# Performance work log

Hardware: AMD Instinct MI355X
Metric: run time of the kernel (lower is better)

The kernel has to match this reference:

```python
import jax, jax.numpy as jnp
import numpy as np

N_NODES = 100_000
N_EDGES = 1_000_000
H = 128
NUM_STATES = 4
UPPER_T, LOWER_T, NUM_ITERS, TEMP_EVAL = 1.0, 0.1, 10000, 0.1


def temp_by_step(step, upper, lower, num_iters, temp_eval):
    # Python-level schedule: eval temp at step == -1, else linear anneal.
    if step == -1:
        return temp_eval
    frac = min(step / num_iters, 1.0)
    return upper + (lower - upper) * frac


def from_binary_states(states):
    # [*, k] bits -> integer id in [0, 2**k)
    weights = 2 ** jnp.arange(states.shape[-1])
    return (states * weights).sum(-1)


def setup_inputs() -> dict:
    key = jax.random.key(0)
    ks = jax.random.split(key, 20)
    N, E, h = N_NODES, N_EDGES, H
    node_states = jax.random.randint(ks[0], (N, NUM_STATES), 0, 2)
    edge_states = jax.random.randint(ks[1], (E, NUM_STATES), 0, 2)
    scalars = jax.random.normal(ks[2], (E, 1), jnp.float32)
    # first N edges are self-loops ordered by node id (required by the module's
    # node_scalars = scalars[src == dst] indexing convention)
    loops = jnp.arange(N)
    src = jax.random.randint(ks[3], (E - N,), 0, N)
    dst = jax.random.randint(ks[4], (E - N,), 0, N)
    dst = jnp.where(dst == src, (dst + 1) % N, dst)  # no accidental self-loops
    edge_index = jnp.stack([jnp.concatenate([loops, src]),
                            jnp.concatenate([loops, dst])])
    batched_reverse_idx = jax.random.randint(ks[5], (E,), 0, E)
    batch_scalars = jax.random.normal(ks[6], (E, 1, 1), jnp.float32)
    s = 0.02
    params = dict(
        node_emb=s * jax.random.normal(ks[7], (2 ** NUM_STATES, h), jnp.float32),
        edge_emb=s * jax.random.normal(ks[8], (2 ** NUM_STATES, h), jnp.float32),
        combine_W=s * jax.random.normal(ks[9], (2 * h, h), jnp.float32),
        combine_b=jnp.zeros((h,), jnp.float32),
        keep_W=s * jax.random.normal(ks[10], (h, 2), jnp.float32),
        keep_b=jnp.zeros((2,), jnp.float32),
        push_W=s * jax.random.normal(ks[11], (h, 2), jnp.float32),
        push_b=jnp.zeros((2,), jnp.float32),
        push_node_W=s * jax.random.normal(ks[12], (h, 2), jnp.float32),
        push_node_b=jnp.zeros((2,), jnp.float32),
        increment_W=s * jax.random.normal(ks[13], (h, 2), jnp.float32),
        increment_b=jnp.zeros((2,), jnp.float32),
    )
    return dict(node_states=node_states, edge_states=edge_states, scalars=scalars,
                edge_index=edge_index, batched_reverse_idx=batched_reverse_idx,
                batch_scalars=batch_scalars, processor_step=0, training_step=0,
                **params)


def reference(node_states, edge_states, scalars, edge_index, batched_reverse_idx,
              batch_scalars, processor_step, training_step,
              node_emb, edge_emb, combine_W, combine_b, keep_W, keep_b,
              push_W, push_b, push_node_W, push_node_b,
              increment_W, increment_b):
    N = node_states.shape[0]
    tau = temp_by_step(int(training_step), UPPER_T, LOWER_T, NUM_ITERS, TEMP_EVAL)
    # use_noise = config.use_noise (False) and training_step != -1 -> False

    node_fts = node_emb[from_binary_states(node_states)]   # [N, h]
    edge_fts = edge_emb[from_binary_states(edge_states)]   # [E, h]
    src, dst = edge_index[0], edge_index[1]
    fts = jnp.concatenate([edge_fts[batched_reverse_idx], node_fts[src]], axis=1)
    fts = fts @ combine_W + combine_b                       # [E, h]

    s = scalars.reshape(-1)                                 # [E]

    def pair_gumbel_first(W, b):
        # grouped (per-edge pair) softmax; take first component (== [::2])
        logits = (fts @ W + b) / tau                        # [E, 2]
        return jax.nn.softmax(logits, axis=-1)[:, 0]

    increment = 1.0 * pair_gumbel_first(increment_W, increment_b)
    keep = s * pair_gumbel_first(keep_W, keep_b)

    # push: first N edges are self-loops, self-loop of node i is edge i
    push_wo = pair_gumbel_first(push_W, push_b)
    push_w = pair_gumbel_first(push_node_W, push_node_b)
    node_scalars = s[:N]                                    # scalars at self-loops
    s_wo = s - node_scalars[dst]
    s_w = s_wo + node_scalars[src]
    acc = (jax.ops.segment_sum(push_wo * s_wo, dst, num_segments=N)
           + jax.ops.segment_sum(push_w * s_w, dst, num_segments=N))  # [N]
    edge_push = jnp.zeros_like(s).at[:N].set(acc)           # nonzero only on self-loops

    new_scalars = (increment + keep + edge_push)[:, None]   # [E, 1]
    target = batch_scalars[:, processor_step]               # [E, 1]
    loss = jnp.mean((target - new_scalars) ** 2)
    return new_scalars, loss
```

## Files before the change

kernel.cpp:

```cpp
#include <hip/hip_runtime.h>
#include <math.h>
#include <stdint.h>

#define N_NODES 100000
#define N_EDGES 1000000
#define N_NONLOOP (N_EDGES - N_NODES)
#define NXCD 8

#define ACC_SCALE   1048576.0f
#define ACC_INV     (1.0f / 1048576.0f)

typedef float  vfloat4 __attribute__((ext_vector_type(4)));
typedef int    vint4   __attribute__((ext_vector_type(4)));

#define XCC_ID_HWREG (20 | ((4 - 1) << 11))

__device__ __forceinline__ int get_xcc() {
    return __builtin_amdgcn_s_getreg(XCC_ID_HWREG) & (NXCD - 1);
}

__device__ __forceinline__ void l2_atomic_add_u32(uint32_t* p, uint32_t v) {
    asm volatile("global_atomic_add %0, %1, off" :: "v"(p), "v"(v) : "memory");
}
__device__ __forceinline__ void l2_atomic_add_f32(float* p, float v) {
    asm volatile("global_atomic_add_f32 %0, %1, off" :: "v"(p), "v"(v) : "memory");
}

__device__ __forceinline__ float get_invtau(const int* __restrict__ training_step) {
    int step = training_step[0];
    float tau;
    if (step == -1) {
        tau = 0.1f;
    } else {
        float frac = fminf((float)step / 10000.0f, 1.0f);
        tau = 1.0f + (0.1f - 1.0f) * frac;
    }
    return 1.0f / tau;
}

__device__ __forceinline__ float wave_reduce(float v) {
    #pragma unroll
    for (int off = 32; off > 0; off >>= 1) v += __shfl_down(v, off, 64);
    return v;
}

#define TAB_BLOCKS  132
#define NODE_BLOCKS 391
#define EI_BLOCKS   977

__global__ __launch_bounds__(256) void fused_pre(
    const int* __restrict__ node_states,
    const int* __restrict__ edge_states,
    const float* __restrict__ node_emb,
    const float* __restrict__ edge_emb,
    const float* __restrict__ cW, const float* __restrict__ cb,
    const float* __restrict__ kW, const float* __restrict__ kb,
    const float* __restrict__ pW, const float* __restrict__ pb,
    const float* __restrict__ pnW, const float* __restrict__ pnb,
    const float* __restrict__ iW, const float* __restrict__ ib,
    const int* __restrict__ tstep,
    uint32_t* __restrict__ acc,
    uint8_t* __restrict__ ei,
    uint8_t* __restrict__ nib,
    float* __restrict__ tabs,
    float* __restrict__ lossp,
    float* __restrict__ loss_out,
    int ncopies)
{
    const int b = blockIdx.x;

    if (b < TAB_BLOCKS) {
        const int w    = b;
        const int lane = threadIdx.x & 63;
        const int wv   = threadIdx.x >> 6;
        const float invtau = get_invtau(tstep);
        __shared__ float part[4];

        float p = 0.f;
        if (w < 128) {
            const int isB = w >> 6, h = (w >> 4) & 3, i = w & 15;
            const float* emb = isB ? node_emb : edge_emb;
            const float* cWh = cW + isB * 128 * 128;
            float t0 = 0.f, t1 = 0.f;
            const int l0 = wv * 32;
            #pragma unroll 8
            for (int l = l0; l < l0 + 32; ++l) {
                const float el = emb[i * 128 + l];
                t0 += el * cWh[l * 128 + lane];
                t1 += el * cWh[l * 128 + 64 + lane];
            }
            const float* W = (h == 0) ? kW : (h == 1) ? pW : (h == 2) ? pnW : iW;
            const float wd0 = W[2 * lane] - W[2 * lane + 1];
            const float wd1 = W[2 * (lane + 64)] - W[2 * (lane + 64) + 1];
            p = t0 * wd0 + t1 * wd1;
        } else if (wv == 0) {
            const int h = w & 3;
            const float* W = (h == 0) ? kW : (h == 1) ? pW : (h == 2) ? pnW : iW;
            const float wd0 = W[2 * lane] - W[2 * lane + 1];
            const float wd1 = W[2 * (lane + 64)] - W[2 * (lane + 64) + 1];
            p = cb[lane] * wd0 + cb[64 + lane] * wd1;
        }
        p = wave_reduce(p);
        if (lane == 0) part[wv] = p;
        __syncthreads();
        if (threadIdx.x == 0) {
            const float tot = part[0] + part[1] + part[2] + part[3];
            if (w < 128) {
                const int isB = w >> 6, h = (w >> 4) & 3, i = w & 15;
                tabs[isB * 64 + i * 4 + h] = tot * invtau;
            } else {
                const int h = w & 3;
                const float* bb = (h == 0) ? kb : (h == 1) ? pb : (h == 2) ? pnb : ib;
                tabs[128 + h] = (tot + bb[0] - bb[1]) * invtau;
            }
        }
        return;
    }

    if (b < TAB_BLOCKS + NODE_BLOCKS) {
        const int n = (b - TAB_BLOCKS) * 256 + threadIdx.x;
        if (n < 256) lossp[n] = 0.f;
        if (n == 0) *loss_out = 0.f;
        if (n < N_NODES) {
            vint4 st = __builtin_nontemporal_load(&((const vint4*)node_states)[n]);
            nib[n] = (uint8_t)(st.x + 2 * st.y + 4 * st.z + 8 * st.w);
            for (int k = 0; k < ncopies; ++k) acc[(size_t)k * N_NODES + n] = 0u;
        }
        return;
    }

    const int t = (b - TAB_BLOCKS - NODE_BLOCKS) * 256 + threadIdx.x;
    if (t < N_EDGES / 4) {
        const vint4* esp = (const vint4*)edge_states + 4 * t;
        vint4 e0 = __builtin_nontemporal_load(esp + 0);
        vint4 e1 = __builtin_nontemporal_load(esp + 1);
        vint4 e2 = __builtin_nontemporal_load(esp + 2);
        vint4 e3 = __builtin_nontemporal_load(esp + 3);
        const uint32_t i0 = e0.x + 2 * e0.y + 4 * e0.z + 8 * e0.w;
        const uint32_t i1 = e1.x + 2 * e1.y + 4 * e1.z + 8 * e1.w;
        const uint32_t i2 = e2.x + 2 * e2.y + 4 * e2.z + 8 * e2.w;
        const uint32_t i3 = e3.x + 2 * e3.y + 4 * e3.z + 8 * e3.w;
        ((uint32_t*)ei)[t] = i0 | (i1 << 8) | (i2 << 16) | (i3 << 24);
    }
}

template<int MODE>
__global__ __launch_bounds__(256) void edge_kernel(
    const float* __restrict__ s,
    const int* __restrict__ src,
    const int* __restrict__ dst,
    const int* __restrict__ brev,
    const uint8_t* __restrict__ ei,
    const uint8_t* __restrict__ nib,
    const float* __restrict__ tabs,
    const float* __restrict__ target,
    uint32_t* __restrict__ acc,
    float* __restrict__ lossp,
    float* __restrict__ out,
    float* __restrict__ loss_out)
{
    __shared__ float4 sf[MODE ? 160 : 33];
    if (threadIdx.x < 33) sf[threadIdx.x] = ((const float4*)tabs)[threadIdx.x];
    __syncthreads();

    int xcc = 0;
    uint32_t* accx = acc;
    if (MODE == 1) {
        xcc  = get_xcc();
        accx = acc + (size_t)xcc * N_NODES;
    }

    const int t = blockIdx.x * blockDim.x + threadIdx.x;
    const bool active = (t < N_NONLOOP / 4);
    float lsum = 0.f;
    float ov[4];
    int   iv[4];
    int   dsv[4];
    int   g = 0;

    if (active) {
        g = (N_NODES / 4) + t;
        const vint4   rv = __builtin_nontemporal_load(&((const vint4*)brev)[g]);
        const vint4   sr = __builtin_nontemporal_load(&((const vint4*)src)[g]);
        const vint4   ds = __builtin_nontemporal_load(&((const vint4*)dst)[g]);
        const vfloat4 sv = __builtin_nontemporal_load(&((const vfloat4*)s)[g]);
        const vfloat4 tg = __builtin_nontemporal_load(&((const vfloat4*)target)[g]);

        const int rvv[4] = {rv.x, rv.y, rv.z, rv.w};
        const int srv[4] = {sr.x, sr.y, sr.z, sr.w};
        dsv[0] = ds.x; dsv[1] = ds.y; dsv[2] = ds.z; dsv[3] = ds.w;
        const float svv[4] = {sv.x, sv.y, sv.z, sv.w};
        const float tgv[4] = {tg.x, tg.y, tg.z, tg.w};

        int   eidx[4], ni[4];
        float ss[4], sd[4];
        #pragma unroll
        for (int j = 0; j < 4; ++j) {
            eidx[j] = ei[rvv[j]];
            ni[j]   = nib[srv[j]];
            ss[j]   = s[srv[j]];
            sd[j]   = s[dsv[j]];
        }

        const float4 c4 = sf[32];
        #pragma unroll
        for (int j = 0; j < 4; ++j) {
            const float4 a = sf[eidx[j]];
            const float4 b = sf[16 + ni[j]];
            const float lk  = a.x + b.x + c4.x;
            const float lp  = a.y + b.y + c4.y;
            const float lpn = a.z + b.z + c4.z;
            const float li  = a.w + b.w + c4.w;
            const float pk  = 1.f / (1.f + __expf(-lk));
            const float pp  = 1.f / (1.f + __expf(-lp));
            const float ppn = 1.f / (1.f + __expf(-lpn));
            const float pi  = 1.f / (1.f + __expf(-li));

            const float s_wo = svv[j] - sd[j];
            const float s_w  = s_wo + ss[j];
            iv[j] = __float2int_rn((pp * s_wo + ppn * s_w) * ACC_SCALE);

            ov[j] = pi + svv[j] * pk;
            const float d = tgv[j] - ov[j];
            lsum += d * d;
        }
    }

    lsum = wave_reduce(lsum);
    __shared__ float wsum[4];
    const int lane = threadIdx.x & 63, wid = threadIdx.x >> 6;
    if (lane == 0) wsum[wid] = lsum;
    __syncthreads();
    if (threadIdx.x == 0) {
        const float tot = (wsum[0] + wsum[1] + wsum[2] + wsum[3]) * (1.0f / (float)N_EDGES);
        if (MODE == 1) l2_atomic_add_f32(&lossp[xcc * 32], tot);
        else           atomicAdd(loss_out, tot);
    }

    if (active) {
        #pragma unroll
        for (int j = 0; j < 4; ++j) {
            if (MODE == 1) l2_atomic_add_u32(&accx[dsv[j]], (uint32_t)iv[j]);
            else           atomicAdd((unsigned int*)&acc[dsv[j]], (unsigned int)iv[j]);
        }
        vfloat4 o4 = {ov[0], ov[1], ov[2], ov[3]};
        __builtin_nontemporal_store(o4, &((vfloat4*)out)[g]);
    }
}

template<int NC>
__global__ __launch_bounds__(256) void finalize_nodes(
    const float* __restrict__ s,
    const int* __restrict__ brev,
    const uint8_t* __restrict__ ei,
    const uint8_t* __restrict__ nib,
    const float* __restrict__ tabs,
    const float* __restrict__ target,
    const uint32_t* __restrict__ acc,
    const float* __restrict__ lossp,
    float* __restrict__ out,
    float* __restrict__ loss_out)
{
    __shared__ float4 sf[33];
    if (threadIdx.x < 33) sf[threadIdx.x] = ((const float4*)tabs)[threadIdx.x];
    __syncthreads();

    const int n = blockIdx.x * blockDim.x + threadIdx.x;
    const bool active = (n < N_NODES);
    float sq = 0.f, v = 0.f;
    if (active) {
        const int  eidx = ei[brev[n]];
        const int  ni   = nib[n];
        const float sv  = s[n];

        uint32_t asum = 0u;
        #pragma unroll
        for (int k = 0; k < NC; ++k) asum += acc[(size_t)k * N_NODES + n];
        const float a8 = (float)(int)asum * ACC_INV;

        const float4 a  = sf[eidx];
        const float4 b  = sf[16 + ni];
        const float4 c4 = sf[32];
        const float lk  = a.x + b.x + c4.x;
        const float lpn = a.z + b.z + c4.z;
        const float li  = a.w + b.w + c4.w;
        const float pk  = 1.f / (1.f + __expf(-lk));
        const float ppn = 1.f / (1.f + __expf(-lpn));
        const float pi  = 1.f / (1.f + __expf(-li));

        v = pi + sv * (pk + ppn) + a8;
        const float d = target[n] - v;
        sq = d * d;
    }
    sq = wave_reduce(sq);
    __shared__ float wsum[4];
    const int lane = threadIdx.x & 63, wid = threadIdx.x >> 6;
    if (lane == 0) wsum[wid] = sq;
    __syncthreads();
    if (threadIdx.x == 0) {
        float tot = (wsum[0] + wsum[1] + wsum[2] + wsum[3]) * (1.0f / (float)N_EDGES);
        if (blockIdx.x == 0) {
            #pragma unroll
            for (int k = 0; k < NXCD; ++k) tot += lossp[k * 32];
        }
        atomicAdd(loss_out, tot);
    }
    if (active) out[n] = v;
}

extern "C" void kernel_launch(void* const* d_in, const int* in_sizes, int n_in,
                              void* d_out, int out_size, void* d_ws, size_t ws_size,
                              hipStream_t stream) {
    const int*   node_states   = (const int*)d_in[0];
    const int*   edge_states   = (const int*)d_in[1];
    const float* scalars       = (const float*)d_in[2];
    const int*   edge_index    = (const int*)d_in[3];
    const int*   brev          = (const int*)d_in[4];
    const float* batch_scalars = (const float*)d_in[5];
    const int*   training_step = (const int*)d_in[7];
    const float* node_emb  = (const float*)d_in[8];
    const float* edge_emb  = (const float*)d_in[9];
    const float* combine_W = (const float*)d_in[10];
    const float* combine_b = (const float*)d_in[11];
    const float* keep_W  = (const float*)d_in[12];
    const float* keep_b  = (const float*)d_in[13];
    const float* push_W  = (const float*)d_in[14];
    const float* push_b  = (const float*)d_in[15];
    const float* pushn_W = (const float*)d_in[16];
    const float* pushn_b = (const float*)d_in[17];
    const float* inc_W   = (const float*)d_in[18];
    const float* inc_b   = (const float*)d_in[19];

    float* out = (float*)d_out;

    const size_t need_scoped = 2048 + (size_t)NXCD * N_NODES * 4 + N_EDGES + N_NODES;
    const bool scoped = (ws_size >= need_scoped);
    const int nc = scoped ? NXCD : 1;

    char* ws = (char*)d_ws;
    float*    tabs  = (float*)ws;
    float*    lossp = (float*)(ws + 1024);
    uint32_t* acc   = (uint32_t*)(ws + 2048);
    uint8_t*  ei    = (uint8_t*)(ws + 2048 + (size_t)nc * N_NODES * 4);
    uint8_t*  nib   = ei + N_EDGES;

    const int* srcp = edge_index;
    const int* dstp = edge_index + N_EDGES;

    fused_pre<<<TAB_BLOCKS + NODE_BLOCKS + EI_BLOCKS, 256, 0, stream>>>(
        node_states, edge_states, node_emb, edge_emb,
        combine_W, combine_b, keep_W, keep_b, push_W, push_b,
        pushn_W, pushn_b, inc_W, inc_b, training_step,
        acc, ei, nib, tabs, lossp, out + N_EDGES, nc);

    const int ethreads = N_NONLOOP / 4;
    const int eblocks  = (ethreads + 255) / 256;
    if (scoped) {
        edge_kernel<1><<<eblocks, 256, 0, stream>>>(
            scalars, srcp, dstp, brev, ei, nib, tabs, batch_scalars,
            acc, lossp, out, out + N_EDGES);
        finalize_nodes<NXCD><<<(N_NODES + 255) / 256, 256, 0, stream>>>(
            scalars, brev, ei, nib, tabs, batch_scalars, acc, lossp, out, out + N_EDGES);
    } else {
        edge_kernel<0><<<eblocks, 256, 0, stream>>>(
            scalars, srcp, dstp, brev, ei, nib, tabs, batch_scalars,
            acc, lossp, out, out + N_EDGES);
        finalize_nodes<1><<<(N_NODES + 255) / 256, 256, 0, stream>>>(
            scalars, brev, ei, nib, tabs, batch_scalars, acc, lossp, out, out + N_EDGES);
    }
}
```

Baseline: 174.6 us.

## Replace global scatter atomics with partitioned binning and LDS accumulation

Instead of fixed-point global atomics into per-XCD accumulator copies, the edge kernel groups each edge's push contribution by destination partition (8 ranges of 12500 nodes). It appends (local index, value) pairs to per-partition buffers using block-level histogram offsets. A new bin_accum kernel accumulates each partition chunk with LDS float atomics into per-block partial rows, and the finalize kernel sums 8 partials per node. This aims to remove contended L2 atomics, at the cost of extra writes and reads of the pair buffer and partials, one more launch, a hard per-partition capacity that silently drops overflow, and a new large workspace requirement; the path only runs if the workspace is big enough.

```diff
diff --git a/kernel.cpp b/kernel.cpp
--- a/kernel.cpp
+++ b/kernel.cpp
@@ -7,18 +7,23 @@
 #define N_NONLOOP (N_EDGES - N_NODES)
 #define NXCD 8
 
+#define NP    8
+#define PSZ   12500
+#define PCAP  120000
+#define GOWN  8
+#define PROW  12544
+
 #define ACC_SCALE   1048576.0f
 #define ACC_INV     (1.0f / 1048576.0f)
 
 typedef float  vfloat4 __attribute__((ext_vector_type(4)));
 typedef int    vint4   __attribute__((ext_vector_type(4)));
+typedef unsigned long long u64;
 
 #define XCC_ID_HWREG (20 | ((4 - 1) << 11))
-
 __device__ __forceinline__ int get_xcc() {
     return __builtin_amdgcn_s_getreg(XCC_ID_HWREG) & (NXCD - 1);
 }
-
 __device__ __forceinline__ void l2_atomic_add_u32(uint32_t* p, uint32_t v) {
     asm volatile("global_atomic_add %0, %1, off" :: "v"(p), "v"(v) : "memory");
 }
@@ -60,6 +65,7 @@
     const float* __restrict__ iW, const float* __restrict__ ib,
     const int* __restrict__ tstep,
     uint32_t* __restrict__ acc,
+    uint32_t* __restrict__ cnt,
     uint8_t* __restrict__ ei,
     uint8_t* __restrict__ nib,
     float* __restrict__ tabs,
@@ -121,6 +127,9 @@
         const int n = (b - TAB_BLOCKS) * 256 + threadIdx.x;
         if (n < 256) lossp[n] = 0.f;
         if (n == 0) *loss_out = 0.f;
+        if (ncopies == 0) {
+            if (n < NP) cnt[n] = 0u;
+        }
         if (n < N_NODES) {
             vint4 st = __builtin_nontemporal_load(&((const vint4*)node_states)[n]);
             nib[n] = (uint8_t)(st.x + 2 * st.y + 4 * st.z + 8 * st.w);
@@ -142,6 +151,201 @@
         const uint32_t i3 = e3.x + 2 * e3.y + 4 * e3.z + 8 * e3.w;
         ((uint32_t*)ei)[t] = i0 | (i1 << 8) | (i2 << 16) | (i3 << 24);
     }
+}
+
+__global__ __launch_bounds__(256) void edge_compact(
+    const float* __restrict__ s,
+    const int* __restrict__ src,
+    const int* __restrict__ dst,
+    const int* __restrict__ brev,
+    const uint8_t* __restrict__ ei,
+    const uint8_t* __restrict__ nib,
+    const float* __restrict__ tabs,
+    const float* __restrict__ target,
+    uint32_t* __restrict__ cnt,
+    u64* __restrict__ pairs,
+    float* __restrict__ lossp,
+    float* __restrict__ out)
+{
+    __shared__ float4 sf[33];
+    __shared__ uint32_t hist[NP], lbase[NP], loff[NP];
+    const int tid = threadIdx.x;
+    if (tid < 33) sf[tid] = ((const float4*)tabs)[tid];
+    if (tid < NP) { hist[tid] = 0u; loff[tid] = 0u; }
+    __syncthreads();
+
+    const int t = blockIdx.x * 256 + tid;
+    const bool active = (t < N_NONLOOP / 4);
+    float lsum = 0.f;
+    float ov[4], av[4];
+    int   pj[4], dloc[4];
+    int   g = 0;
+
+    if (active) {
+        g = (N_NODES / 4) + t;
+        const vint4   rv = __builtin_nontemporal_load(&((const vint4*)brev)[g]);
+        const vint4   sr = __builtin_nontemporal_load(&((const vint4*)src)[g]);
+        const vint4   ds = __builtin_nontemporal_load(&((const vint4*)dst)[g]);
+        const vfloat4 sv = __builtin_nontemporal_load(&((const vfloat4*)s)[g]);
+        const vfloat4 tg = __builtin_nontemporal_load(&((const vfloat4*)target)[g]);
+
+        const int rvv[4] = {rv.x, rv.y, rv.z, rv.w};
+        const int srv[4] = {sr.x, sr.y, sr.z, sr.w};
+        const int dsv[4] = {ds.x, ds.y, ds.z, ds.w};
+        const float svv[4] = {sv.x, sv.y, sv.z, sv.w};
+        const float tgv[4] = {tg.x, tg.y, tg.z, tg.w};
+
+        int   eidx[4], ni[4];
+        float ss[4], sd[4];
+        #pragma unroll
+        for (int j = 0; j < 4; ++j) {
+            eidx[j] = ei[rvv[j]];
+            ni[j]   = nib[srv[j]];
+            ss[j]   = s[srv[j]];
+            sd[j]   = s[dsv[j]];
+        }
+
+        const float4 c4 = sf[32];
+        #pragma unroll
+        for (int j = 0; j < 4; ++j) {
+            const float4 a = sf[eidx[j]];
+            const float4 b = sf[16 + ni[j]];
+            const float lk  = a.x + b.x + c4.x;
+            const float lp  = a.y + b.y + c4.y;
+            const float lpn = a.z + b.z + c4.z;
+            const float li  = a.w + b.w + c4.w;
+            const float pk  = 1.f / (1.f + __expf(-lk));
+            const float pp  = 1.f / (1.f + __expf(-lp));
+            const float ppn = 1.f / (1.f + __expf(-lpn));
+            const float pi  = 1.f / (1.f + __expf(-li));
+
+            const float s_wo = svv[j] - sd[j];
+            const float s_w  = s_wo + ss[j];
+            av[j] = pp * s_wo + ppn * s_w;
+
+            const uint32_t p = (uint32_t)dsv[j] / 12500u;
+            pj[j]   = (int)p;
+            dloc[j] = dsv[j] - (int)p * 12500;
+
+            ov[j] = pi + svv[j] * pk;
+            const float d = tgv[j] - ov[j];
+            lsum += d * d;
+        }
+        #pragma unroll
+        for (int j = 0; j < 4; ++j) atomicAdd(&hist[pj[j]], 1u);
+    }
+
+    __syncthreads();
+    if (tid < NP) lbase[tid] = atomicAdd(&cnt[tid], hist[tid]);
+    __syncthreads();
+
+    if (active) {
+        #pragma unroll
+        for (int j = 0; j < 4; ++j) {
+            const uint32_t k    = atomicAdd(&loff[pj[j]], 1u);
+            const uint32_t slot = lbase[pj[j]] + k;
+            if (slot < PCAP)
+                pairs[(size_t)pj[j] * PCAP + slot] =
+                    ((u64)(uint32_t)dloc[j] << 32) | (uint32_t)__float_as_int(av[j]);
+        }
+        vfloat4 o4 = {ov[0], ov[1], ov[2], ov[3]};
+        __builtin_nontemporal_store(o4, &((vfloat4*)out)[g]);
+    }
+
+    lsum = wave_reduce(lsum);
+    if ((tid & 63) == 0)
+        atomicAdd(&lossp[(blockIdx.x & 15) * 16], lsum);
+}
+
+__global__ __launch_bounds__(256) void bin_accum(
+    const u64* __restrict__ pairs,
+    const uint32_t* __restrict__ cnt,
+    float* __restrict__ partials)
+{
+    __shared__ float part[PSZ];
+    const int tid = threadIdx.x;
+    const int p = blockIdx.x >> 3, r = blockIdx.x & 7;
+
+    for (int k = tid; k < PSZ; k += 256) part[k] = 0.f;
+    __syncthreads();
+
+    uint32_t c = cnt[p];
+    if (c > PCAP) c = PCAP;
+    const uint32_t chunk = (c + GOWN - 1) / GOWN;
+    const uint32_t lo = r * chunk;
+    uint32_t hi = lo + chunk;
+    if (hi > c) hi = c;
+
+    const u64* pp = pairs + (size_t)p * PCAP;
+    for (uint32_t i = lo + tid; i < hi; i += 256) {
+        const u64 v = pp[i];
+        atomicAdd(&part[(uint32_t)(v >> 32)], __int_as_float((int)(uint32_t)v));
+    }
+    __syncthreads();
+
+    float* row = partials + (size_t)blockIdx.x * PROW;
+    for (int k = tid; k < PSZ; k += 256) row[k] = part[k];
+}
+
+__global__ __launch_bounds__(256) void finalize_binned(
+    const float* __restrict__ s,
+    const int* __restrict__ brev,
+    const uint8_t* __restrict__ ei,
+    const uint8_t* __restrict__ nib,
+    const float* __restrict__ tabs,
+    const float* __restrict__ target,
+    const float* __restrict__ partials,
+    const float* __restrict__ lossp,
+    float* __restrict__ out,
+    float* __restrict__ loss_out)
+{
+    __shared__ float4 sf[33];
+    if (threadIdx.x < 33) sf[threadIdx.x] = ((const float4*)tabs)[threadIdx.x];
+    __syncthreads();
+
+    const int n = blockIdx.x * blockDim.x + threadIdx.x;
+    const bool active = (n < N_NODES);
+    float sq = 0.f, v = 0.f;
+    if (active) {
+        const int  eidx = ei[brev[n]];
+        const int  ni   = nib[n];
+        const float sv  = s[n];
+
+        const uint32_t p   = (uint32_t)n / 12500u;
+        const uint32_t off = (uint32_t)n - p * 12500u;
+        const float* pr = partials + (size_t)p * GOWN * PROW + off;
+        float a8 = 0.f;
+        #pragma unroll
+        for (int r = 0; r < GOWN; ++r) a8 += pr[(size_t)r * PROW];
+
+        const float4 a  = sf[eidx];
+        const float4 b  = sf[16 + ni];
+        const float4 c4 = sf[32];
+        const float lk  = a.x + b.x + c4.x;
+        const float lpn = a.z + b.z + c4.z;
+        const float li  = a.w + b.w + c4.w;
+        const float pk  = 1.f / (1.f + __expf(-lk));
+        const float ppn = 1.f / (1.f + __expf(-lpn));
+        const float pi  = 1.f / (1.f + __expf(-li));
+
+        v = pi + sv * (pk + ppn) + a8;
+        const float d = target[n] - v;
+        sq = d * d;
+    }
+    sq = wave_reduce(sq);
+    __shared__ float wsum[4];
+    const int lane = threadIdx.x & 63, wid = threadIdx.x >> 6;
+    if (lane == 0) wsum[wid] = sq;
+    __syncthreads();
+    if (threadIdx.x == 0) {
+        float tot = (wsum[0] + wsum[1] + wsum[2] + wsum[3]) * (1.0f / (float)N_EDGES);
+        if (blockIdx.x == 0) {
+            #pragma unroll
+            for (int c = 0; c < 16; ++c) tot += lossp[c * 16] * (1.0f / (float)N_EDGES);
+        }
+        atomicAdd(loss_out, tot);
+    }
+    if (active) out[n] = v;
 }
 
 template<int MODE>
@@ -333,39 +537,72 @@
 
     float* out = (float*)d_out;
 
-    const size_t need_scoped = 2048 + (size_t)NXCD * N_NODES * 4 + N_EDGES + N_NODES;
-    const bool scoped = (ws_size >= need_scoped);
-    const int nc = scoped ? NXCD : 1;
-
-    char* ws = (char*)d_ws;
-    float*    tabs  = (float*)ws;
-    float*    lossp = (float*)(ws + 1024);
-    uint32_t* acc   = (uint32_t*)(ws + 2048);
-    uint8_t*  ei    = (uint8_t*)(ws + 2048 + (size_t)nc * N_NODES * 4);
-    uint8_t*  nib   = ei + N_EDGES;
-
     const int* srcp = edge_index;
     const int* dstp = edge_index + N_EDGES;
 
-    fused_pre<<<TAB_BLOCKS + NODE_BLOCKS + EI_BLOCKS, 256, 0, stream>>>(
-        node_states, edge_states, node_emb, edge_emb,
-        combine_W, combine_b, keep_W, keep_b, push_W, push_b,
-        pushn_W, pushn_b, inc_W, inc_b, training_step,
-        acc, ei, nib, tabs, lossp, out + N_EDGES, nc);
-
+    const size_t PAIRS_B    = (size_t)NP * PCAP * 8;
+    const size_t PARTIALS_B = (size_t)NP * GOWN * PROW * 4;
+    const size_t need_binned = 3072 + PAIRS_B + PARTIALS_B + N_EDGES + N_NODES;
+    const size_t need_scoped = 2048 + (size_t)NXCD * N_NODES * 4 + N_EDGES + N_NODES;
+
+    char* ws = (char*)d_ws;
     const int ethreads = N_NONLOOP / 4;
     const int eblocks  = (ethreads + 255) / 256;
-    if (scoped) {
-        edge_kernel<1><<<eblocks, 256, 0, stream>>>(
+
+    if (ws_size >= need_binned) {
+        float*    tabs     = (float*)ws;
+        float*    lossp    = (float*)(ws + 1024);
+        uint32_t* cnt      = (uint32_t*)(ws + 2048);
+        u64*      pairs    = (u64*)(ws + 3072);
+        float*    partials = (float*)(ws + 3072 + PAIRS_B);
+        uint8_t*  ei       = (uint8_t*)(ws + 3072 + PAIRS_B + PARTIALS_B);
+        uint8_t*  nib      = ei + N_EDGES;
+
+        fused_pre<<<TAB_BLOCKS + NODE_BLOCKS + EI_BLOCKS, 256, 0, stream>>>(
+            node_states, edge_states, node_emb, edge_emb,
+            combine_W, combine_b, keep_W, keep_b, push_W, push_b,
+            pushn_W, pushn_b, inc_W, inc_b, training_step,
+            nullptr, cnt, ei, nib, tabs, lossp, out + N_EDGES, 0);
+
+        edge_compact<<<eblocks, 256, 0, stream>>>(
             scalars, srcp, dstp, brev, ei, nib, tabs, batch_scalars,
-            acc, lossp, out, out + N_EDGES);
-        finalize_nodes<NXCD><<<(N_NODES + 255) / 256, 256, 0, stream>>>(
-            scalars, brev, ei, nib, tabs, batch_scalars, acc, lossp, out, out + N_EDGES);
+            cnt, pairs, lossp, out);
+
+        bin_accum<<<NP * GOWN, 256, 0, stream>>>(pairs, cnt, partials);
+
+        finalize_binned<<<(N_NODES + 255) / 256, 256, 0, stream>>>(
+            scalars, brev, ei, nib, tabs, batch_scalars, partials, lossp,
+            out, out + N_EDGES);
     } else {
-        edge_kernel<0><<<eblocks, 256, 0, stream>>>(
-            scalars, srcp, dstp, brev, ei, nib, tabs, batch_scalars,
-            acc, lossp, out, out + N_EDGES);
-        finalize_nodes<1><<<(N_NODES + 255) / 256, 256, 0, stream>>>(
-            scalars, brev, ei, nib, tabs, batch_scalars, acc, lossp, out, out + N_EDGES);
-    }
-}
+        const bool scoped = (ws_size >= need_scoped);
+        const int nc = scoped ? NXCD : 1;
+
+        float*    tabs  = (float*)ws;
+        float*    lossp = (float*)(ws + 1024);
+        uint32_t* acc   = (uint32_t*)(ws + 2048);
+        uint8_t*  ei    = (uint8_t*)(ws + 2048 + (size_t)nc * N_NODES * 4);
+        uint8_t*  nib   = ei + N_EDGES;
+
+        fused_pre<<<TAB_BLOCKS + NODE_BLOCKS + EI_BLOCKS, 256, 0, stream>>>(
+            node_states, edge_states, node_emb, edge_emb,
+            combine_W, combine_b, keep_W, keep_b, push_W, push_b,
+            pushn_W, pushn_b, inc_W, inc_b, training_step,
+            acc, nullptr, ei, nib, tabs, lossp, out + N_EDGES, nc);
+
+        if (scoped) {
+            edge_kernel<1><<<eblocks, 256, 0, stream>>>(
+                scalars, srcp, dstp, brev, ei, nib, tabs, batch_scalars,
+                acc, lossp, out, out + N_EDGES);
+            finalize_nodes<NXCD><<<(N_NODES + 255) / 256, 256, 0, stream>>>(
+                scalars, brev, ei, nib, tabs, batch_scalars, acc, lossp,
+                out, out + N_EDGES);
+        } else {
+            edge_kernel<0><<<eblocks, 256, 0, stream>>>(
+                scalars, srcp, dstp, brev, ei, nib, tabs, batch_scalars,
+                acc, lossp, out, out + N_EDGES);
+            finalize_nodes<1><<<(N_NODES + 255) / 256, 256, 0, stream>>>(
+                scalars, brev, ei, nib, tabs, batch_scalars, acc, lossp,
+                out, out + N_EDGES);
+        }
+    }
+}
```

After: 170.2 us. -2.5%, faster.
